# Performance work log

Measured on AMD Instinct MI355X. Metric: run time of the kernel, lower is better.

## Reference

```python
import jax, jax.numpy as jnp
import numpy as np

N_HEAD = 16
NEG = -1.0e9


def setup_inputs() -> dict:
    key = jax.random.key(0)
    k1, k2, k3 = jax.random.split(key, 3)
    B, T, C = 4, 2048, 1024
    x = jax.random.normal(k1, (B, T, C), dtype=jnp.float32)
    # torch Linear(C, 3C, bias=False): weight [3C, C], y = x @ W.T
    w_attn = jax.random.normal(k2, (3 * C, C), dtype=jnp.float32) * (1.0 / np.sqrt(C))
    w_proj = jax.random.normal(k3, (C, C), dtype=jnp.float32) * (1.0 / np.sqrt(C))
    return {"x": x, "w_attn": w_attn, "w_proj": w_proj}


def reference(x, w_attn, w_proj):
    B, T, C = x.shape
    hd = C // N_HEAD
    qkv = x @ w_attn.T  # [B,T,3C]
    q, k, v = jnp.split(qkv, 3, axis=2)
    # [B,T,C] -> [B,H,T,hd]
    q = q.reshape(B, T, N_HEAD, hd).transpose(0, 2, 1, 3)
    k = k.reshape(B, T, N_HEAD, hd).transpose(0, 2, 1, 3)
    v = v.reshape(B, T, N_HEAD, hd).transpose(0, 2, 1, 3)
    att = jnp.einsum('bhqd,bhkd->bhqk', q, k) * (1.0 / np.sqrt(hd))
    causal = jnp.tril(jnp.ones((T, T), dtype=bool))
    att = jnp.where(causal[None, None, :, :], att, NEG)
    att = jax.nn.softmax(att, axis=-1)
    y = jnp.einsum('bhqk,bhkd->bhqd', att, v)  # [B,H,T,hd]
    y = y.transpose(0, 2, 1, 3).reshape(B, T, C)
    return y @ w_proj.T
```

## Files before the change

### kernel.cpp

```cpp
#include <hip/hip_runtime.h>
#include <hip/hip_bf16.h>

typedef __bf16 bf16x8_t __attribute__((ext_vector_type(8)));
typedef __bf16 bf16x4_t __attribute__((ext_vector_type(4)));
typedef float f32x4_t __attribute__((ext_vector_type(4)));

__device__ __forceinline__ void gload_lds16(const void* g, void* l) {
    __builtin_amdgcn_global_load_lds((const __attribute__((address_space(1))) void*)g,
                                     (__attribute__((address_space(3))) void*)l, 16, 0, 0);
}

__global__ void f2bf_kernel(const float* __restrict__ in, __bf16* __restrict__ out, int n) {
    int i = (blockIdx.x * blockDim.x + threadIdx.x) * 4;
    if (i >= n) return;
    float4 v = *(const float4*)(in + i);
    bf16x4_t o;
    o[0] = (__bf16)v.x; o[1] = (__bf16)v.y; o[2] = (__bf16)v.z; o[3] = (__bf16)v.w;
    *(bf16x4_t*)(out + i) = o;
}

__global__ __launch_bounds__(512, 2) void gemm1_8ph(const __bf16* __restrict__ A,
                                                    const __bf16* __restrict__ Bt,
                                                    __bf16* __restrict__ Cqk,
                                                    __bf16* __restrict__ Vg,
                                                    int M, int N, int K) {
    __shared__ __bf16 AsB[2][16 * 512];
    __shared__ __bf16 BsB[2][32 * 512];

    const int tid  = threadIdx.x;
    const int lane = tid & 63;
    const int wid  = tid >> 6;
    const int wm   = wid >> 2;
    const int wn   = wid & 3;

    const int nwg   = gridDim.x;
    const int ntile = N >> 8;
    int fl = blockIdx.x;
    fl = (fl & 7) * (nwg >> 3) + (fl >> 3);
    const int m0 = (fl / ntile) * 128;
    const int n0 = (fl % ntile) * 256;

    const int lr = lane & 15;
    const int lg = lane >> 4;
    const int cr = lg * 4;
    const int srow = lane >> 3;
    const int gcol = (((lane & 7) ^ srow) << 3);

    f32x4_t acc[4][4];
#pragma unroll
    for (int i = 0; i < 4; ++i)
#pragma unroll
        for (int j = 0; j < 4; ++j)
            acc[i][j] = (f32x4_t){0.f, 0.f, 0.f, 0.f};

    const int NT = K >> 6;

    auto stage = [&](int kt, int buf) {
        const __bf16* Ab = A + (size_t)m0 * K + kt * 64;
        const __bf16* Bb = Bt + (size_t)n0 * K + kt * 64;
        __bf16* Al = &AsB[buf][0];
        __bf16* Bl = &BsB[buf][0];
#pragma unroll
        for (int j = 0; j < 6; ++j) {
            int seg = wid * 6 + j;
            if (seg < 16) {
                gload_lds16(Ab + (size_t)(seg * 8 + srow) * K + gcol, Al + seg * 512);
            } else {
                int s2 = seg - 16;
                gload_lds16(Bb + (size_t)(s2 * 8 + srow) * K + gcol, Bl + s2 * 512);
            }
        }
    };

    stage(0, 0);

    for (int kt = 0; kt < NT; ++kt) {
        const int cur = kt & 1;
        const bool pf = (kt + 1 < NT);
        if (pf) stage(kt + 1, cur ^ 1);

        if (pf) asm volatile("s_waitcnt vmcnt(6)" ::: "memory");
        else    asm volatile("s_waitcnt vmcnt(0)" ::: "memory");
        __builtin_amdgcn_sched_barrier(0);
        __builtin_amdgcn_s_barrier();
        __builtin_amdgcn_sched_barrier(0);

        const __bf16* Al = &AsB[cur][0];
        const __bf16* Bl = &BsB[cur][0];

        bf16x8_t af[4][2];
#pragma unroll
        for (int mf = 0; mf < 4; ++mf)
#pragma unroll
            for (int kk = 0; kk < 2; ++kk) {
                const int row = wm * 64 + mf * 16 + lr;
                const int g   = kk * 4 + lg;
                af[mf][kk] = *(const bf16x8_t*)&Al[row * 64 + ((g ^ (row & 7)) << 3)];
            }

#pragma unroll
        for (int p = 0; p < 2; ++p) {
            bf16x8_t bfr[2][2];
#pragma unroll
            for (int nfp = 0; nfp < 2; ++nfp)
#pragma unroll
                for (int kk = 0; kk < 2; ++kk) {
                    const int row = wn * 64 + (p * 2 + nfp) * 16 + lr;
                    const int g   = kk * 4 + lg;
                    bfr[nfp][kk] = *(const bf16x8_t*)&Bl[row * 64 + ((g ^ (row & 7)) << 3)];
                }
            __builtin_amdgcn_s_setprio(1);
#pragma unroll
            for (int mf = 0; mf < 4; ++mf)
#pragma unroll
                for (int nfp = 0; nfp < 2; ++nfp) {
                    const int nf = p * 2 + nfp;
                    acc[mf][nf] = __builtin_amdgcn_mfma_f32_16x16x32_bf16(af[mf][0], bfr[nfp][0], acc[mf][nf], 0, 0, 0);
                    acc[mf][nf] = __builtin_amdgcn_mfma_f32_16x16x32_bf16(af[mf][1], bfr[nfp][1], acc[mf][nf], 0, 0, 0);
                }
            __builtin_amdgcn_s_setprio(0);
            __builtin_amdgcn_s_barrier();
        }
        __builtin_amdgcn_sched_barrier(0);
    }

    if (n0 < 2048) {
#pragma unroll
        for (int mf = 0; mf < 4; ++mf)
#pragma unroll
            for (int nf = 0; nf < 4; ++nf)
#pragma unroll
                for (int r = 0; r < 4; ++r) {
                    int row = m0 + wm * 64 + mf * 16 + cr + r;
                    int col = n0 + wn * 64 + nf * 16 + lr;
                    Cqk[(size_t)row * 2048 + col] = (__bf16)acc[mf][nf][r];
                }
    } else {
#pragma unroll
        for (int mf = 0; mf < 4; ++mf) {
            const int row0 = m0 + wm * 64 + mf * 16 + cr;
            const int bb   = row0 >> 11;
            const int tt   = row0 & 2047;
#pragma unroll
            for (int nf = 0; nf < 4; ++nf) {
                const int c3 = n0 + wn * 64 + nf * 16 + lr - 2048;
                const int hh = c3 >> 6, dd = c3 & 63;
                bf16x4_t pv;
#pragma unroll
                for (int r = 0; r < 4; ++r) pv[r] = (__bf16)acc[mf][nf][r];
                *(bf16x4_t*)&Vg[((size_t)(bb * 16 + hh) * 64 + dd) * 2048 + tt] = pv;
            }
        }
    }
}

template <typename OutT>
__global__ __launch_bounds__(256) void gemm_bt(const __bf16* __restrict__ A,
                                               const __bf16* __restrict__ Bt,
                                               OutT* __restrict__ C,
                                               int M, int N, int K) {
    __shared__ __bf16 As[128 * 32];
    __shared__ __bf16 Bs[128 * 32];

    const int tid  = threadIdx.x;
    const int lane = tid & 63;
    const int wid  = tid >> 6;
    const int wm   = wid >> 1;
    const int wn   = wid & 1;

    const int nwg = gridDim.x * gridDim.y;
    int fl = blockIdx.y * gridDim.x + blockIdx.x;
    fl = (fl & 7) * (nwg >> 3) + (fl >> 3);
    const int m0 = (fl / gridDim.x) * 128;
    const int n0 = (fl % gridDim.x) * 128;

    const int lr = lane & 15;
    const int lk = (lane >> 4) * 8;
    const int cr = (lane >> 4) * 4;

    f32x4_t acc[4][4];
    for (int i = 0; i < 4; ++i)
        for (int j = 0; j < 4; ++j)
            acc[i][j] = (f32x4_t){0.f, 0.f, 0.f, 0.f};

    for (int k0 = 0; k0 < K; k0 += 32) {
        __syncthreads();
        for (int i = 0; i < 2; ++i) {
            int flat = i * 256 + tid;
            int row  = flat >> 2;
            int col  = (flat & 3) * 8;
            gload_lds16(&A[(size_t)(m0 + row) * K + k0 + col], &As[(size_t)(i * 256 + wid * 64) * 8]);
            gload_lds16(&Bt[(size_t)(n0 + row) * K + k0 + col], &Bs[(size_t)(i * 256 + wid * 64) * 8]);
        }
        __syncthreads();

        bf16x8_t af[4], bfr[4];
        for (int mf = 0; mf < 4; ++mf)
            af[mf] = *(const bf16x8_t*)&As[(wm * 64 + mf * 16 + lr) * 32 + lk];
        for (int nf = 0; nf < 4; ++nf)
            bfr[nf] = *(const bf16x8_t*)&Bs[(wn * 64 + nf * 16 + lr) * 32 + lk];
        for (int mf = 0; mf < 4; ++mf)
            for (int nf = 0; nf < 4; ++nf)
                acc[mf][nf] = __builtin_amdgcn_mfma_f32_16x16x32_bf16(af[mf], bfr[nf], acc[mf][nf], 0, 0, 0);
    }

    for (int mf = 0; mf < 4; ++mf)
        for (int nf = 0; nf < 4; ++nf)
            for (int r = 0; r < 4; ++r) {
                int row = m0 + wm * 64 + mf * 16 + cr + r;
                int col = n0 + wn * 64 + nf * 16 + lr;
                C[(size_t)row * N + col] = (OutT)acc[mf][nf][r];
            }
}

__global__ __launch_bounds__(512, 4) void attn_kernel(const __bf16* __restrict__ qkv,
                                                      const __bf16* __restrict__ Vg,
                                                      __bf16* __restrict__ y) {
    const int T = 2048, LD = 2048;
    const int orig = blockIdx.x;
    const int bidx = ((orig & 7) << 6) + (orig >> 3);
    const int pair = bidx & 7;
    const int h    = (bidx >> 3) & 15;
    const int b    = bidx >> 7;

    __shared__ __bf16 Ks[128 * 64];
    __shared__ __bf16 Vt[64 * 128];
    __shared__ __bf16 Ps[8 * 16 * 136];

    const int tid  = threadIdx.x;
    const int lane = tid & 63;
    const int w    = tid >> 6;
    const int lr   = lane & 15;
    const int lg   = lane >> 4;
    const int lk   = lg * 8;

    const __bf16* qg  = qkv + (size_t)b * T * LD + h * 64;
    const __bf16* kg  = qg + 1024;
    const __bf16* Vgb = Vg + (size_t)(b * 16 + h) * 64 * 2048;

    const float CE    = 0.125f * 1.44269504f;
    const float DEFER = 44.0f;

    const int r0    = tid >> 3;
    const int kcol  = (tid & 7) * 8;
    const int kslot = ((tid & 7) ^ (r0 & 7)) << 3;
    const int vd  = tid >> 3;
    const int vc0 = tid & 7;

    __bf16* Pw = &Ps[w * 16 * 136];

    for (int pass = 0; pass < 2; ++pass) {
        const int qs  = pass ? 15 - pair : pair;
        const int qt0 = qs * 128;
        const int nt  = qs + 1;

        bf16x8_t qf0, qf1;
        {
            const __bf16* qrow = qg + (size_t)(qt0 + w * 16 + lr) * LD;
            qf0 = *(const bf16x8_t*)&qrow[lk];
            qf1 = *(const bf16x8_t*)&qrow[32 + lk];
        }

        bf16x8_t ka = *(const bf16x8_t*)&kg[(size_t)r0 * LD + kcol];
        bf16x8_t kb = *(const bf16x8_t*)&kg[(size_t)(64 + r0) * LD + kcol];
        bf16x8_t va = *(const bf16x8_t*)&Vgb[(size_t)vd * 2048 + vc0 * 8];
        bf16x8_t vb = *(const bf16x8_t*)&Vgb[(size_t)vd * 2048 + (vc0 + 8) * 8];

        f32x4_t o_acc[4];
#pragma unroll
        for (int i = 0; i < 4; ++i) o_acc[i] = (f32x4_t){0.f, 0.f, 0.f, 0.f};
        float m_r = -3.0e38f, l_r = 0.f;

        for (int t = 0; t < nt; ++t) {
            __syncthreads();

            *(bf16x8_t*)&Ks[r0 * 64 + kslot] = ka;
            *(bf16x8_t*)&Ks[(64 + r0) * 64 + kslot] = kb;
            *(bf16x8_t*)&Vt[vd * 128 + ((vc0 ^ (vd & 7)) << 3)] = va;
            *(bf16x8_t*)&Vt[vd * 128 + (((vc0 + 8) ^ (vd & 7)) << 3)] = vb;

            __syncthreads();

            if (t + 1 < nt) {
                const size_t kb0 = (size_t)(t + 1) * 128;
                ka = *(const bf16x8_t*)&kg[(kb0 + r0) * LD + kcol];
                kb = *(const bf16x8_t*)&kg[(kb0 + 64 + r0) * LD + kcol];
                va = *(const bf16x8_t*)&Vgb[(size_t)vd * 2048 + kb0 + vc0 * 8];
                vb = *(const bf16x8_t*)&Vgb[(size_t)vd * 2048 + kb0 + (vc0 + 8) * 8];
            }

            f32x4_t s[8];
#pragma unroll
            for (int c = 0; c < 8; ++c) {
                const int key = c * 16 + lr;
                const int sw  = (key & 7) << 3;
                bf16x8_t kfa = *(const bf16x8_t*)&Ks[key * 64 + (lk ^ sw)];
                bf16x8_t kfb = *(const bf16x8_t*)&Ks[key * 64 + ((32 + lk) ^ sw)];
                s[c] = __builtin_amdgcn_mfma_f32_16x16x32_bf16(kfa, qf0, (f32x4_t){0.f, 0.f, 0.f, 0.f}, 0, 0, 0);
                s[c] = __builtin_amdgcn_mfma_f32_16x16x32_bf16(kfb, qf1, s[c], 0, 0, 0);
            }

            if (t == nt - 1) {
                const int ql = w * 16 + lr;
#pragma unroll
                for (int c = 0; c < 8; ++c)
#pragma unroll
                    for (int r = 0; r < 4; ++r)
                        if (c * 16 + lg * 4 + r > ql) s[c][r] = -1.0e30f;
            }

            float pm = s[0][0];
#pragma unroll
            for (int c = 0; c < 8; ++c)
#pragma unroll
                for (int r = 0; r < 4; ++r) pm = fmaxf(pm, s[c][r]);

            if (!__all(pm <= m_r + DEFER)) {
                pm = fmaxf(pm, __shfl_xor(pm, 16));
                pm = fmaxf(pm, __shfl_xor(pm, 32));
                const float mn    = fmaxf(m_r, pm);
                const float alpha = exp2f((m_r - mn) * CE);
                l_r *= alpha;
#pragma unroll
                for (int dt = 0; dt < 4; ++dt)
#pragma unroll
                    for (int r = 0; r < 4; ++r) o_acc[dt][r] *= alpha;
                m_r = mn;
            }
            const float mce = m_r * CE;

            float rs = 0.f;
#pragma unroll
            for (int c = 0; c < 8; ++c) {
                bf16x4_t pk;
#pragma unroll
                for (int r = 0; r < 4; ++r) {
                    float pv = exp2f(fmaf(s[c][r], CE, -mce));
                    rs += pv;
                    pk[r] = (__bf16)pv;
                }
                *(bf16x4_t*)&Pw[lr * 136 + c * 16 + lg * 4] = pk;
            }
            rs += __shfl_xor(rs, 16);
            rs += __shfl_xor(rs, 32);
            l_r += rs;

#pragma unroll
            for (int hf = 0; hf < 2; ++hf) {
                bf16x8_t pb0 = *(const bf16x8_t*)&Pw[lr * 136 + hf * 64 + lk];
                bf16x8_t pb1 = *(const bf16x8_t*)&Pw[lr * 136 + hf * 64 + 32 + lk];
#pragma unroll
                for (int dt = 0; dt < 4; ++dt) {
                    const int d = dt * 16 + lr;
                    bf16x8_t vb0 = *(const bf16x8_t*)&Vt[d * 128 + (((hf * 8 + lg) ^ (d & 7)) << 3)];
                    bf16x8_t vb1 = *(const bf16x8_t*)&Vt[d * 128 + (((hf * 8 + 4 + lg) ^ (d & 7)) << 3)];
                    o_acc[dt] = __builtin_amdgcn_mfma_f32_16x16x32_bf16(vb0, pb0, o_acc[dt], 0, 0, 0);
                    o_acc[dt] = __builtin_amdgcn_mfma_f32_16x16x32_bf16(vb1, pb1, o_acc[dt], 0, 0, 0);
                }
            }
        }

        const float inv = 1.0f / l_r;
        const int q = qt0 + w * 16 + lr;
#pragma unroll
        for (int dt = 0; dt < 4; ++dt) {
            bf16x4_t ov;
#pragma unroll
            for (int r = 0; r < 4; ++r) ov[r] = (__bf16)(o_acc[dt][r] * inv);
            *(bf16x4_t*)&y[(size_t)(b * T + q) * 1024 + h * 64 + dt * 16 + lg * 4] = ov;
        }
    }
}

extern "C" void kernel_launch(void* const* d_in, const int* in_sizes, int n_in,
                              void* d_out, int out_size, void* d_ws, size_t ws_size,
                              hipStream_t stream) {
    const float* x      = (const float*)d_in[0];
    const float* w_attn = (const float*)d_in[1];
    const float* w_proj = (const float*)d_in[2];
    float* out = (float*)d_out;

    char* ws = (char*)d_ws;
    __bf16* xb   = (__bf16*)(ws);
    __bf16* wab  = (__bf16*)(ws + 16777216);
    __bf16* wpb  = (__bf16*)(ws + 23068672);
    __bf16* qkvb = (__bf16*)(ws + 25165824);
    __bf16* yb   = (__bf16*)(ws + 58720256);
    __bf16* Vg   = (__bf16*)(ws + 75497472);

    f2bf_kernel<<<8192, 256, 0, stream>>>(x, xb, 8388608);
    f2bf_kernel<<<3072, 256, 0, stream>>>(w_attn, wab, 3145728);
    f2bf_kernel<<<1024, 256, 0, stream>>>(w_proj, wpb, 1048576);

    gemm1_8ph<<<768, 512, 0, stream>>>(xb, wab, qkvb, Vg, 8192, 3072, 1024);

    attn_kernel<<<512, 512, 0, stream>>>(qkvb, Vg, yb);

    gemm_bt<float><<<dim3(8, 64), 256, 0, stream>>>(yb, wpb, out, 8192, 1024, 1024);
}
```

Before: 188.2 us.

## Enlarge QKV GEMM tile to 256x256 with interleaved 8-phase pipeline, fuse converts

The QKV GEMM moves from 128x256 to 256x256 tiles with double-buffered LDS. It uses a hand-scheduled 8-phase loop that interleaves half-tile global-to-LDS loads with MFMA sub-blocks, raising arithmetic intensity per LDS byte. The three fp32-to-bf16 conversion launches are merged into one kernel. Attention MFMA sections get raised wave priority. The larger tile uses 128KB of LDS, which limits occupancy to one block per CU, and the grid of 384 blocks leaves a partial wave.

```diff
diff --git a/kernel.cpp b/kernel.cpp
--- a/kernel.cpp
+++ b/kernel.cpp
@@ -10,22 +10,27 @@
                                      (__attribute__((address_space(3))) void*)l, 16, 0, 0);
 }
 
-__global__ void f2bf_kernel(const float* __restrict__ in, __bf16* __restrict__ out, int n) {
-    int i = (blockIdx.x * blockDim.x + threadIdx.x) * 4;
-    if (i >= n) return;
-    float4 v = *(const float4*)(in + i);
+__global__ void f2bf3_kernel(const float* __restrict__ x, const float* __restrict__ wa,
+                             const float* __restrict__ wp, __bf16* __restrict__ xb,
+                             __bf16* __restrict__ wab, __bf16* __restrict__ wpb) {
+    int i = blockIdx.x * blockDim.x + threadIdx.x;
+    const float* in; __bf16* out; int off;
+    if (i < 2097152)      { in = x;  out = xb;  off = i; }
+    else if (i < 2883584) { in = wa; out = wab; off = i - 2097152; }
+    else                  { in = wp; out = wpb; off = i - 2883584; }
+    float4 v = *(const float4*)(in + off * 4);
     bf16x4_t o;
     o[0] = (__bf16)v.x; o[1] = (__bf16)v.y; o[2] = (__bf16)v.z; o[3] = (__bf16)v.w;
-    *(bf16x4_t*)(out + i) = o;
-}
-
-__global__ __launch_bounds__(512, 2) void gemm1_8ph(const __bf16* __restrict__ A,
-                                                    const __bf16* __restrict__ Bt,
-                                                    __bf16* __restrict__ Cqk,
-                                                    __bf16* __restrict__ Vg,
-                                                    int M, int N, int K) {
-    __shared__ __bf16 AsB[2][16 * 512];
-    __shared__ __bf16 BsB[2][32 * 512];
+    *(bf16x4_t*)(out + off * 4) = o;
+}
+
+__global__ __launch_bounds__(512, 2) void gemm1_m201(const __bf16* __restrict__ A,
+                                                     const __bf16* __restrict__ Bt,
+                                                     __bf16* __restrict__ Cqk,
+                                                     __bf16* __restrict__ Vg,
+                                                     int M, int N, int K) {
+    __shared__ __bf16 As[2][256 * 64];
+    __shared__ __bf16 Bs[2][256 * 64];
 
     const int tid  = threadIdx.x;
     const int lane = tid & 63;
@@ -33,12 +38,10 @@
     const int wm   = wid >> 2;
     const int wn   = wid & 3;
 
-    const int nwg   = gridDim.x;
-    const int ntile = N >> 8;
     int fl = blockIdx.x;
-    fl = (fl & 7) * (nwg >> 3) + (fl >> 3);
-    const int m0 = (fl / ntile) * 128;
-    const int n0 = (fl % ntile) * 256;
+    fl = (fl & 7) * (gridDim.x >> 3) + (fl >> 3);
+    const int m0 = (fl / 12) * 256;
+    const int n0 = (fl % 12) * 256;
 
     const int lr = lane & 15;
     const int lg = lane >> 4;
@@ -46,99 +49,143 @@
     const int srow = lane >> 3;
     const int gcol = (((lane & 7) ^ srow) << 3);
 
-    f32x4_t acc[4][4];
-#pragma unroll
-    for (int i = 0; i < 4; ++i)
+    f32x4_t acc[8][4];
+#pragma unroll
+    for (int i = 0; i < 8; ++i)
 #pragma unroll
         for (int j = 0; j < 4; ++j)
             acc[i][j] = (f32x4_t){0.f, 0.f, 0.f, 0.f};
 
     const int NT = K >> 6;
-
-    auto stage = [&](int kt, int buf) {
-        const __bf16* Ab = A + (size_t)m0 * K + kt * 64;
-        const __bf16* Bb = Bt + (size_t)n0 * K + kt * 64;
-        __bf16* Al = &AsB[buf][0];
-        __bf16* Bl = &BsB[buf][0];
-#pragma unroll
-        for (int j = 0; j < 6; ++j) {
-            int seg = wid * 6 + j;
-            if (seg < 16) {
-                gload_lds16(Ab + (size_t)(seg * 8 + srow) * K + gcol, Al + seg * 512);
-            } else {
-                int s2 = seg - 16;
-                gload_lds16(Bb + (size_t)(s2 * 8 + srow) * K + gcol, Bl + s2 * 512);
-            }
-        }
+    const int NI = NT >> 1;
+
+    bf16x8_t af[4][2], bf0[2][2], bf1[2][2];
+
+    auto stA = [&](int kt, int buf, int half) {
+        const __bf16* Ab = A + (size_t)m0 * K + (size_t)kt * 64;
+        const int s0 = half * 16 + wid, s1 = s0 + 8;
+        gload_lds16(Ab + (size_t)(s0 * 8 + srow) * K + gcol, &As[buf][s0 * 512]);
+        gload_lds16(Ab + (size_t)(s1 * 8 + srow) * K + gcol, &As[buf][s1 * 512]);
     };
-
-    stage(0, 0);
-
-    for (int kt = 0; kt < NT; ++kt) {
-        const int cur = kt & 1;
-        const bool pf = (kt + 1 < NT);
-        if (pf) stage(kt + 1, cur ^ 1);
-
-        if (pf) asm volatile("s_waitcnt vmcnt(6)" ::: "memory");
-        else    asm volatile("s_waitcnt vmcnt(0)" ::: "memory");
-        __builtin_amdgcn_sched_barrier(0);
-        __builtin_amdgcn_s_barrier();
-        __builtin_amdgcn_sched_barrier(0);
-
-        const __bf16* Al = &AsB[cur][0];
-        const __bf16* Bl = &BsB[cur][0];
-
-        bf16x8_t af[4][2];
+    auto stB = [&](int kt, int buf, int half) {
+        const __bf16* Bb = Bt + (size_t)n0 * K + (size_t)kt * 64;
+        const int s0 = half * 16 + wid, s1 = s0 + 8;
+        gload_lds16(Bb + (size_t)(s0 * 8 + srow) * K + gcol, &Bs[buf][s0 * 512]);
+        gload_lds16(Bb + (size_t)(s1 * 8 + srow) * K + gcol, &Bs[buf][s1 * 512]);
+    };
+    auto dsA = [&](const __bf16* Ab, int mfh) {
 #pragma unroll
         for (int mf = 0; mf < 4; ++mf)
 #pragma unroll
             for (int kk = 0; kk < 2; ++kk) {
-                const int row = wm * 64 + mf * 16 + lr;
+                const int row = wm * 128 + (mfh * 4 + mf) * 16 + lr;
                 const int g   = kk * 4 + lg;
-                af[mf][kk] = *(const bf16x8_t*)&Al[row * 64 + ((g ^ (row & 7)) << 3)];
-            }
-
-#pragma unroll
-        for (int p = 0; p < 2; ++p) {
-            bf16x8_t bfr[2][2];
-#pragma unroll
-            for (int nfp = 0; nfp < 2; ++nfp)
-#pragma unroll
-                for (int kk = 0; kk < 2; ++kk) {
-                    const int row = wn * 64 + (p * 2 + nfp) * 16 + lr;
-                    const int g   = kk * 4 + lg;
-                    bfr[nfp][kk] = *(const bf16x8_t*)&Bl[row * 64 + ((g ^ (row & 7)) << 3)];
-                }
-            __builtin_amdgcn_s_setprio(1);
-#pragma unroll
-            for (int mf = 0; mf < 4; ++mf)
-#pragma unroll
-                for (int nfp = 0; nfp < 2; ++nfp) {
-                    const int nf = p * 2 + nfp;
-                    acc[mf][nf] = __builtin_amdgcn_mfma_f32_16x16x32_bf16(af[mf][0], bfr[nfp][0], acc[mf][nf], 0, 0, 0);
-                    acc[mf][nf] = __builtin_amdgcn_mfma_f32_16x16x32_bf16(af[mf][1], bfr[nfp][1], acc[mf][nf], 0, 0, 0);
-                }
-            __builtin_amdgcn_s_setprio(0);
-            __builtin_amdgcn_s_barrier();
-        }
-        __builtin_amdgcn_sched_barrier(0);
+                af[mf][kk] = *(const bf16x8_t*)&Ab[row * 64 + ((g ^ (row & 7)) << 3)];
+            }
+    };
+    auto dsB = [&](const __bf16* Bb, int nfh, bf16x8_t (&dst)[2][2]) {
+#pragma unroll
+        for (int nfp = 0; nfp < 2; ++nfp)
+#pragma unroll
+            for (int kk = 0; kk < 2; ++kk) {
+                const int row = wn * 64 + (nfh * 2 + nfp) * 16 + lr;
+                const int g   = kk * 4 + lg;
+                dst[nfp][kk] = *(const bf16x8_t*)&Bb[row * 64 + ((g ^ (row & 7)) << 3)];
+            }
+    };
+    auto MF = [&](int mfh, bf16x8_t (&bfr)[2][2], int nfh) {
+        __builtin_amdgcn_s_setprio(1);
+#pragma unroll
+        for (int mf = 0; mf < 4; ++mf)
+#pragma unroll
+            for (int nfp = 0; nfp < 2; ++nfp) {
+                const int ai = mfh * 4 + mf, bi = nfh * 2 + nfp;
+                acc[ai][bi] = __builtin_amdgcn_mfma_f32_16x16x32_bf16(af[mf][0], bfr[nfp][0], acc[ai][bi], 0, 0, 0);
+                acc[ai][bi] = __builtin_amdgcn_mfma_f32_16x16x32_bf16(af[mf][1], bfr[nfp][1], acc[ai][bi], 0, 0, 0);
+            }
+        __builtin_amdgcn_s_setprio(0);
+    };
+
+#define BAR() __builtin_amdgcn_s_barrier()
+#define LGK0() asm volatile("s_waitcnt lgkmcnt(0)" ::: "memory")
+
+    stA(0, 0, 0); stA(0, 0, 1); stB(0, 0, 0); stB(0, 0, 1);
+    stB(1, 1, 0); stB(1, 1, 1);
+    asm volatile("s_waitcnt vmcnt(4)" ::: "memory");
+    BAR();
+
+    for (int it = 0; it < NI; ++it) {
+        const int t1 = 2 * it + 1, t2 = 2 * it + 2, t3 = 2 * it + 3;
+        const bool lastit = (it == NI - 1);
+
+        dsA(As[0], 0); dsB(Bs[0], 0, bf0);
+        stA(t1, 1, 0);
+        BAR(); LGK0();
+        MF(0, bf0, 0);
+        BAR();
+
+        dsB(Bs[0], 1, bf1);
+        stA(t1, 1, 1);
+        BAR(); LGK0();
+        MF(0, bf1, 1);
+        BAR();
+
+        dsA(As[0], 1);
+        if (!lastit) stB(t2, 0, 0);
+        BAR(); LGK0();
+        MF(1, bf0, 0);
+        BAR();
+
+        if (!lastit) stB(t2, 0, 1);
+        if (lastit) asm volatile("s_waitcnt vmcnt(0)" ::: "memory");
+        else        asm volatile("s_waitcnt vmcnt(4)" ::: "memory");
+        BAR();
+        MF(1, bf1, 1);
+        BAR();
+
+        dsA(As[1], 0); dsB(Bs[1], 0, bf0);
+        if (!lastit) stA(t2, 0, 0);
+        BAR(); LGK0();
+        MF(0, bf0, 0);
+        BAR();
+
+        dsB(Bs[1], 1, bf1);
+        if (!lastit) stA(t2, 0, 1);
+        BAR(); LGK0();
+        MF(0, bf1, 1);
+        BAR();
+
+        dsA(As[1], 1);
+        if (!lastit) stB(t3, 1, 0);
+        BAR(); LGK0();
+        MF(1, bf0, 0);
+        BAR();
+
+        if (!lastit) stB(t3, 1, 1);
+        if (lastit) asm volatile("s_waitcnt vmcnt(0)" ::: "memory");
+        else        asm volatile("s_waitcnt vmcnt(4)" ::: "memory");
+        BAR();
+        MF(1, bf1, 1);
+        BAR();
     }
+#undef BAR
+#undef LGK0
 
     if (n0 < 2048) {
 #pragma unroll
-        for (int mf = 0; mf < 4; ++mf)
+        for (int mf = 0; mf < 8; ++mf)
 #pragma unroll
             for (int nf = 0; nf < 4; ++nf)
 #pragma unroll
                 for (int r = 0; r < 4; ++r) {
-                    int row = m0 + wm * 64 + mf * 16 + cr + r;
+                    int row = m0 + wm * 128 + mf * 16 + cr + r;
                     int col = n0 + wn * 64 + nf * 16 + lr;
                     Cqk[(size_t)row * 2048 + col] = (__bf16)acc[mf][nf][r];
                 }
     } else {
 #pragma unroll
-        for (int mf = 0; mf < 4; ++mf) {
-            const int row0 = m0 + wm * 64 + mf * 16 + cr;
+        for (int mf = 0; mf < 8; ++mf) {
+            const int row0 = m0 + wm * 128 + mf * 16 + cr;
             const int bb   = row0 >> 11;
             const int tt   = row0 & 2047;
 #pragma unroll
@@ -290,6 +337,7 @@
             }
 
             f32x4_t s[8];
+            __builtin_amdgcn_s_setprio(1);
 #pragma unroll
             for (int c = 0; c < 8; ++c) {
                 const int key = c * 16 + lr;
@@ -299,6 +347,7 @@
                 s[c] = __builtin_amdgcn_mfma_f32_16x16x32_bf16(kfa, qf0, (f32x4_t){0.f, 0.f, 0.f, 0.f}, 0, 0, 0);
                 s[c] = __builtin_amdgcn_mfma_f32_16x16x32_bf16(kfb, qf1, s[c], 0, 0, 0);
             }
+            __builtin_amdgcn_s_setprio(0);
 
             if (t == nt - 1) {
                 const int ql = w * 16 + lr;
@@ -345,6 +394,7 @@
             rs += __shfl_xor(rs, 32);
             l_r += rs;
 
+            __builtin_amdgcn_s_setprio(1);
 #pragma unroll
             for (int hf = 0; hf < 2; ++hf) {
                 bf16x8_t pb0 = *(const bf16x8_t*)&Pw[lr * 136 + hf * 64 + lk];
@@ -358,6 +408,7 @@
                     o_acc[dt] = __builtin_amdgcn_mfma_f32_16x16x32_bf16(vb1, pb1, o_acc[dt], 0, 0, 0);
                 }
             }
+            __builtin_amdgcn_s_setprio(0);
         }
 
         const float inv = 1.0f / l_r;
@@ -388,11 +439,9 @@
     __bf16* yb   = (__bf16*)(ws + 58720256);
     __bf16* Vg   = (__bf16*)(ws + 75497472);
 
-    f2bf_kernel<<<8192, 256, 0, stream>>>(x, xb, 8388608);
-    f2bf_kernel<<<3072, 256, 0, stream>>>(w_attn, wab, 3145728);
-    f2bf_kernel<<<1024, 256, 0, stream>>>(w_proj, wpb, 1048576);
-
-    gemm1_8ph<<<768, 512, 0, stream>>>(xb, wab, qkvb, Vg, 8192, 3072, 1024);
+    f2bf3_kernel<<<12288, 256, 0, stream>>>(x, w_attn, w_proj, xb, wab, wpb);
+
+    gemm1_m201<<<384, 512, 0, stream>>>(xb, wab, qkvb, Vg, 8192, 3072, 1024);
 
     attn_kernel<<<512, 512, 0, stream>>>(qkvb, Vg, yb);
 
```

New measurement: 181.3 us. 3.7% less time.
